# Optimization experiments

Hardware: AMD Instinct MI355X
Metric: run time of the kernel (lower is better)

Reference implementation:

```python
import jax, jax.numpy as jnp
import numpy as np

N_NODES = 50000
N_EDGES = 800000
NUM_GRAPHS = 1024
IN_DIM = 25
DIM = 64
STEPS = 3


def setup_inputs() -> dict:
    key = jax.random.key(0)
    ks = jax.random.split(key, 16)
    s = 0.1
    return {
        "x": jax.random.normal(ks[0], (N_NODES, IN_DIM), dtype=jnp.float32),
        "edge_index": jax.random.randint(ks[1], (2, N_EDGES), 0, N_NODES),
        "batch": jnp.sort(jax.random.randint(ks[2], (N_NODES,), 0, NUM_GRAPHS)),
        "W0": jax.random.normal(ks[3], (IN_DIM, DIM), dtype=jnp.float32) * s,
        "b0": jnp.zeros((DIM,), jnp.float32),
        "Wc": jax.random.normal(ks[4], (DIM, DIM), dtype=jnp.float32) * s,
        "bc": jnp.zeros((DIM,), jnp.float32),
        "Wih": jax.random.normal(ks[5], (4 * DIM, 2 * DIM), dtype=jnp.float32) * s,
        "Whh": jax.random.normal(ks[6], (4 * DIM, DIM), dtype=jnp.float32) * s,
        "bih": jnp.zeros((4 * DIM,), jnp.float32),
        "bhh": jnp.zeros((4 * DIM,), jnp.float32),
        "W1": jax.random.normal(ks[7], (2 * DIM, DIM), dtype=jnp.float32) * s,
        "b1": jnp.zeros((DIM,), jnp.float32),
        "W2": jax.random.normal(ks[8], (DIM, 1), dtype=jnp.float32) * s,
        "b2": jnp.zeros((1,), jnp.float32),
    }


def _lstm_cell(xin, h, c, Wih, Whh, bih, bhh):
    gates = xin @ Wih.T + h @ Whh.T + bih + bhh  # [B, 4*DIM]
    i, f, g, o = jnp.split(gates, 4, axis=-1)
    i, f, o = jax.nn.sigmoid(i), jax.nn.sigmoid(f), jax.nn.sigmoid(o)
    g = jnp.tanh(g)
    c = f * c + i * g
    h = o * jnp.tanh(c)
    return h, c


def reference(x, edge_index, batch, W0, b0, Wc, bc, Wih, Whh, bih, bhh, W1, b1, W2, b2):
    n = x.shape[0]
    # lin0 + relu
    h = jax.nn.relu(x @ W0 + b0)
    # GCNConv: x @ W, add self loops, symmetric normalization, scatter-add
    hw = h @ Wc
    loops = jnp.arange(n, dtype=edge_index.dtype)
    row = jnp.concatenate([edge_index[0], loops])  # sources
    col = jnp.concatenate([edge_index[1], loops])  # targets
    deg = jax.ops.segment_sum(jnp.ones_like(row, dtype=hw.dtype), col, num_segments=n)
    dinv = jnp.where(deg > 0, jax.lax.rsqrt(deg), 0.0)
    norm = dinv[row] * dinv[col]
    msg = hw[row] * norm[:, None]  # [E+N, DIM] gather
    agg = jax.ops.segment_sum(msg, col, num_segments=n) + bc
    h = jax.nn.relu(agg)
    # Set2Set pooling with LSTM, 3 processing steps
    B = NUM_GRAPHS
    q_star = jnp.zeros((B, 2 * DIM), h.dtype)
    hs = jnp.zeros((B, DIM), h.dtype)
    cs = jnp.zeros((B, DIM), h.dtype)
    for _ in range(STEPS):
        hs, cs = _lstm_cell(q_star, hs, cs, Wih, Whh, bih, bhh)
        q = hs  # [B, DIM]
        e = jnp.sum(h * q[batch], axis=-1)  # [N]
        emax = jax.ops.segment_max(e, batch, num_segments=B)
        a = jnp.exp(e - emax[batch])
        asum = jax.ops.segment_sum(a, batch, num_segments=B)
        a = a / asum[batch]
        r = jax.ops.segment_sum(a[:, None] * h, batch, num_segments=B)  # [B, DIM]
        q_star = jnp.concatenate([q, r], axis=-1)
    out = jax.nn.relu(q_star @ W1 + b1)
    out = out @ W2 + b2
    return out.reshape(-1)
```

## Files before the change

### kernel.cpp

```cpp
#include <hip/hip_runtime.h>
#include <hip/hip_fp16.h>
#include <math.h>

#define N_NODES 50000
#define N_EDGES 800000
#define NGRAPH  1024
#define IN_DIM  25
#define DIM     64

#define NBKB 782
#define CAP  1536
#define NBIN 391
#define CROWS 128

__device__ inline float wsum(float v) {
#pragma unroll
  for (int off = 32; off > 0; off >>= 1) v += __shfl_xor(v, off, 64);
  return v;
}
__device__ inline float sigmoidf(float x) { return 1.f / (1.f + expf(-x)); }

__global__ __launch_bounds__(256) void k_bin(const int* __restrict__ ei,
    int* __restrict__ gcur, int* __restrict__ pairs,
    const float* __restrict__ Wih, const float* __restrict__ Whh,
    float* __restrict__ WT) {
  __shared__ int hist[NBKB];
  __shared__ int sbase[NBKB];
  __shared__ int lbase[NBKB];
  __shared__ int sorted[2048];
  int t = threadIdx.x;
  if (blockIdx.x == NBIN) {
    for (int i = t; i < 3 * DIM * 4 * DIM; i += 256) {
      int k = i >> 8, tt = i & 255;
      WT[i] = (k < 2 * DIM) ? Wih[tt * 2 * DIM + k] : Whh[tt * DIM + (k - 2 * DIM)];
    }
    return;
  }
  int base = blockIdx.x * 2048;
  for (int i = t; i < NBKB; i += 256) hist[i] = 0;
  __syncthreads();
  int pk[8], bkt[8], rank[8];
#pragma unroll
  for (int k = 0; k < 8; k++) {
    int e = base + k * 256 + t;
    if (e < N_EDGES) {
      int row = ei[e];
      int col = ei[N_EDGES + e];
      int b = col >> 6;
      bkt[k] = b;
      rank[k] = atomicAdd(&hist[b], 1);
      pk[k] = (int)(((unsigned)b << 22) | ((unsigned)(col & 63) << 16) | (unsigned)row);
    } else {
      bkt[k] = -1;
    }
  }
  __syncthreads();
  if (t < 64) {
    int v[13];
    int loc = 0;
#pragma unroll
    for (int i = 0; i < 13; i++) {
      int idx = t * 13 + i;
      v[i] = (idx < NBKB) ? hist[idx] : 0;
      loc += v[i];
    }
    int x = loc;
#pragma unroll
    for (int d = 1; d < 64; d <<= 1) {
      int y = __shfl_up(x, d, 64);
      if (t >= d) x += y;
    }
    int excl = x - loc;
#pragma unroll
    for (int i = 0; i < 13; i++) {
      int idx = t * 13 + i;
      if (idx < NBKB) sbase[idx] = excl;
      excl += v[i];
    }
  }
  __syncthreads();
#pragma unroll
  for (int k = 0; k < 8; k++)
    if (bkt[k] >= 0) sorted[sbase[bkt[k]] + rank[k]] = pk[k];
  for (int i = t; i < NBKB; i += 256)
    lbase[i] = hist[i] ? atomicAdd(&gcur[i], hist[i]) : 0;
  __syncthreads();
  int ntot = min(2048, N_EDGES - base);
  for (int i = t; i < ntot; i += 256) {
    int p = sorted[i];
    int b = ((unsigned)p) >> 22;
    int gpos = lbase[b] + (i - sbase[b]);
    if (gpos < CAP) pairs[(size_t)b * CAP + gpos] = p & 0x3FFFFF;
  }
}

__global__ __launch_bounds__(256) void k_lin0(const float* __restrict__ x,
    const float* __restrict__ W0, const float* __restrict__ b0,
    const float* __restrict__ Wc, const int* __restrict__ pairs,
    const int* __restrict__ gcur, float* __restrict__ dinv,
    __half* __restrict__ hw16) {
  __shared__ float sx[64][IN_DIM + 1];
  __shared__ float sW0[IN_DIM][DIM];
  __shared__ float sh[64][DIM + 4];
  __shared__ float sWc[DIM][DIM];
  __shared__ int histd[64];
  int t = threadIdx.x;
  int row0 = blockIdx.x * 64;
  if (t < 64) histd[t] = 0;
  __syncthreads();
  for (int i = t; i < 64 * IN_DIM; i += 256) {
    int r = i / IN_DIM, k = i - r * IN_DIM;
    int row = row0 + r;
    sx[r][k] = (row < N_NODES) ? x[row * IN_DIM + k] : 0.f;
  }
  for (int i = t; i < IN_DIM * DIM; i += 256) sW0[i >> 6][i & 63] = W0[i];
  for (int i = t; i < DIM * DIM; i += 256) sWc[i >> 6][i & 63] = Wc[i];
  {
    int ne = min(gcur[blockIdx.x], CAP);
    const int* pp = pairs + (size_t)blockIdx.x * CAP;
    const int4* pp4 = (const int4*)pp;
    int ne4 = ne >> 2;
    for (int i = t; i < ne4; i += 256) {
      int4 p4 = pp4[i];
      atomicAdd(&histd[(p4.x >> 16) & 63], 1);
      atomicAdd(&histd[(p4.y >> 16) & 63], 1);
      atomicAdd(&histd[(p4.z >> 16) & 63], 1);
      atomicAdd(&histd[(p4.w >> 16) & 63], 1);
    }
    for (int i = (ne4 << 2) + t; i < ne; i += 256)
      atomicAdd(&histd[(pp[i] >> 16) & 63], 1);
  }
  __syncthreads();
  int tc = (t & 15) * 4;
  int tr = (t >> 4) * 4;
  float acc[4][4];
  {
    float4 bb = *(const float4*)&b0[tc];
#pragma unroll
    for (int i = 0; i < 4; i++) {
      acc[i][0] = bb.x; acc[i][1] = bb.y; acc[i][2] = bb.z; acc[i][3] = bb.w;
    }
  }
#pragma unroll
  for (int k = 0; k < IN_DIM; k++) {
    float4 w = *(const float4*)&sW0[k][tc];
#pragma unroll
    for (int i = 0; i < 4; i++) {
      float a = sx[tr + i][k];
      acc[i][0] += a * w.x; acc[i][1] += a * w.y;
      acc[i][2] += a * w.z; acc[i][3] += a * w.w;
    }
  }
#pragma unroll
  for (int i = 0; i < 4; i++) {
    sh[tr + i][tc + 0] = fmaxf(acc[i][0], 0.f);
    sh[tr + i][tc + 1] = fmaxf(acc[i][1], 0.f);
    sh[tr + i][tc + 2] = fmaxf(acc[i][2], 0.f);
    sh[tr + i][tc + 3] = fmaxf(acc[i][3], 0.f);
  }
  __syncthreads();
#pragma unroll
  for (int i = 0; i < 4; i++) acc[i][0] = acc[i][1] = acc[i][2] = acc[i][3] = 0.f;
#pragma unroll 8
  for (int k = 0; k < DIM; k++) {
    float4 w = *(const float4*)&sWc[k][tc];
#pragma unroll
    for (int i = 0; i < 4; i++) {
      float a = sh[tr + i][k];
      acc[i][0] += a * w.x; acc[i][1] += a * w.y;
      acc[i][2] += a * w.z; acc[i][3] += a * w.w;
    }
  }
  if (t < 64) {
    int node = row0 + t;
    if (node < N_NODES) dinv[node] = rsqrtf((float)(histd[t] + 1));
  }
  float2* hwf2 = (float2*)hw16;
#pragma unroll
  for (int i = 0; i < 4; i++) {
    int row = row0 + tr + i;
    if (row < N_NODES) {
      float dv = rsqrtf((float)(histd[tr + i] + 1));
      float2 st;
      ((__half2*)&st)[0] = __floats2half2_rn(acc[i][0] * dv, acc[i][1] * dv);
      ((__half2*)&st)[1] = __floats2half2_rn(acc[i][2] * dv, acc[i][3] * dv);
      hwf2[(size_t)row * 16 + (t & 15)] = st;
    }
  }
}

__global__ __launch_bounds__(256) void k_agg(const int* __restrict__ pairs,
    const int* __restrict__ gcur, const __half* __restrict__ hw16,
    const float* __restrict__ dinv, const float4* __restrict__ bc4,
    __half* __restrict__ h16) {
  __shared__ unsigned short rows[CAP];
  __shared__ int hist[64];
  __shared__ int off[65];
  __shared__ int cur[64];
  int b = blockIdx.x, t = threadIdx.x;
  int lane = t & 63, wave = t >> 6, q = lane >> 4, ql = lane & 15;
  int qid = (wave << 2) + q;
  if (t < 64) hist[t] = 0;
  __syncthreads();
  int ne = min(gcur[b], CAP);
  const int* pp = pairs + (size_t)b * CAP;
  const int4* pp4 = (const int4*)pp;
  int ne4 = ne >> 2;
  for (int i = t; i < ne4; i += 256) {
    int4 p4 = pp4[i];
    atomicAdd(&hist[(p4.x >> 16) & 63], 1);
    atomicAdd(&hist[(p4.y >> 16) & 63], 1);
    atomicAdd(&hist[(p4.z >> 16) & 63], 1);
    atomicAdd(&hist[(p4.w >> 16) & 63], 1);
  }
  for (int i = (ne4 << 2) + t; i < ne; i += 256)
    atomicAdd(&hist[(pp[i] >> 16) & 63], 1);
  __syncthreads();
  if (t < 64) {
    int v = hist[t];
    int x = v;
#pragma unroll
    for (int d = 1; d < 64; d <<= 1) {
      int y = __shfl_up(x, d, 64);
      if (t >= d) x += y;
    }
    off[t] = x - v;
    cur[t] = x - v;
    if (t == 63) off[64] = x;
  }
  __syncthreads();
  for (int i = t; i < ne4; i += 256) {
    int4 p4 = pp4[i];
#pragma unroll
    for (int u = 0; u < 4; u++) {
      int p = (&p4.x)[u];
      int slot = atomicAdd(&cur[(p >> 16) & 63], 1);
      rows[slot] = (unsigned short)(p & 0xFFFF);
    }
  }
  for (int i = (ne4 << 2) + t; i < ne; i += 256) {
    int p = pp[i];
    int slot = atomicAdd(&cur[(p >> 16) & 63], 1);
    rows[slot] = (unsigned short)(p & 0xFFFF);
  }
  __syncthreads();
  const float2* hwf2 = (const float2*)hw16;
  float4 bb = bc4[ql];
  for (int nl = qid; nl < 64; nl += 16) {
    int node = b * 64 + nl;
    if (node >= N_NODES) continue;
    int s0 = off[nl], e0 = off[nl + 1];
    float4 a0, a1, a2, a3;
    {
      float2 raw = hwf2[(size_t)node * 16 + ql];
      float2 f0 = __half22float2(((const __half2*)&raw)[0]);
      float2 f1 = __half22float2(((const __half2*)&raw)[1]);
      a0 = make_float4(f0.x, f0.y, f1.x, f1.y);
      a1 = make_float4(0.f, 0.f, 0.f, 0.f); a2 = a1; a3 = a1;
    }
    int j = s0;
    for (; j + 4 <= e0; j += 4) {
      int r0 = rows[j], r1 = rows[j + 1], r2 = rows[j + 2], r3 = rows[j + 3];
      float2 w0 = hwf2[(size_t)r0 * 16 + ql];
      float2 w1 = hwf2[(size_t)r1 * 16 + ql];
      float2 w2 = hwf2[(size_t)r2 * 16 + ql];
      float2 w3 = hwf2[(size_t)r3 * 16 + ql];
      float2 f;
      f = __half22float2(((const __half2*)&w0)[0]); a0.x += f.x; a0.y += f.y;
      f = __half22float2(((const __half2*)&w0)[1]); a0.z += f.x; a0.w += f.y;
      f = __half22float2(((const __half2*)&w1)[0]); a1.x += f.x; a1.y += f.y;
      f = __half22float2(((const __half2*)&w1)[1]); a1.z += f.x; a1.w += f.y;
      f = __half22float2(((const __half2*)&w2)[0]); a2.x += f.x; a2.y += f.y;
      f = __half22float2(((const __half2*)&w2)[1]); a2.z += f.x; a2.w += f.y;
      f = __half22float2(((const __half2*)&w3)[0]); a3.x += f.x; a3.y += f.y;
      f = __half22float2(((const __half2*)&w3)[1]); a3.z += f.x; a3.w += f.y;
    }
    for (; j < e0; j++) {
      int r = rows[j];
      float2 w = hwf2[(size_t)r * 16 + ql];
      float2 f;
      f = __half22float2(((const __half2*)&w)[0]); a0.x += f.x; a0.y += f.y;
      f = __half22float2(((const __half2*)&w)[1]); a0.z += f.x; a0.w += f.y;
    }
    float di = dinv[node];
    float ox = fmaxf(((a0.x + a1.x) + (a2.x + a3.x)) * di + bb.x, 0.f);
    float oy = fmaxf(((a0.y + a1.y) + (a2.y + a3.y)) * di + bb.y, 0.f);
    float oz = fmaxf(((a0.z + a1.z) + (a2.z + a3.z)) * di + bb.z, 0.f);
    float ow = fmaxf(((a0.w + a1.w) + (a2.w + a3.w)) * di + bb.w, 0.f);
    float2 st;
    ((__half2*)&st)[0] = __floats2half2_rn(ox, oy);
    ((__half2*)&st)[1] = __floats2half2_rn(oz, ow);
    ((float2*)h16)[(size_t)node * 16 + ql] = st;
  }
}

__global__ __launch_bounds__(256) void k_set2set(
    const __half* __restrict__ h16, const int* __restrict__ batch,
    const float* __restrict__ WT, const float* __restrict__ bih,
    const float* __restrict__ bhh, const float* __restrict__ W1,
    const float* __restrict__ b1, const float* __restrict__ W2,
    const float* __restrict__ b2, float* __restrict__ out) {
  int b = blockIdx.x, t = threadIdx.x;
  int wave = t >> 6, lane = t & 63;
  int q = lane >> 4, ql = lane & 15;
  int qid = (wave << 2) + q;
  __shared__ float2 hcf2[CROWS * 16];
  __shared__ float qs[2 * DIM];
  __shared__ float hsl[DIM], csl[DIM];
  __shared__ float gates[4 * DIM];
  __shared__ float red[16 * DIM];
  __shared__ float lred[16], wmax[16];
  __shared__ int seg[2];
  const float2* h2 = (const float2*)h16;
  if (t < 2) {
    int g = b + t;
    int lo = 0, hi = N_NODES;
    if (g == NGRAPH) lo = N_NODES;
    else while (lo < hi) { int mid = (lo + hi) >> 1; if (batch[mid] < g) lo = mid + 1; else hi = mid; }
    seg[t] = lo;
  }
  if (t < 2 * DIM) qs[t] = 0.f;
  if (t < DIM) { hsl[t] = 0.f; csl[t] = 0.f; }
  __syncthreads();
  int s = seg[0], eend = seg[1];
  int nc = min(eend - s, CROWS);
  for (int i = t; i < nc * 16; i += 256)
    hcf2[i] = h2[(size_t)(s + (i >> 4)) * 16 + (i & 15)];
  __syncthreads();
  float bsum = bih[t] + bhh[t];
  for (int step = 0; step < 3; step++) {
    float g = bsum;
    if (step > 0) {
      const float* wp = WT + t;
      float g1 = 0.f;
#pragma unroll 8
      for (int k = 0; k < 2 * DIM; k += 2) {
        g += qs[k] * wp[k * 4 * DIM];
        g1 += qs[k + 1] * wp[(k + 1) * 4 * DIM];
      }
#pragma unroll 8
      for (int k = 0; k < DIM; k += 2) {
        g += hsl[k] * wp[(2 * DIM + k) * 4 * DIM];
        g1 += hsl[k + 1] * wp[(2 * DIM + k + 1) * 4 * DIM];
      }
      g += g1;
    }
    gates[t] = g;
    __syncthreads();
    if (t < DIM) {
      float ig = sigmoidf(gates[t]);
      float fg = sigmoidf(gates[DIM + t]);
      float gg = tanhf(gates[2 * DIM + t]);
      float og = sigmoidf(gates[3 * DIM + t]);
      float c = fg * csl[t] + ig * gg;
      csl[t] = c;
      float hh = og * tanhf(c);
      hsl[t] = hh;
      qs[t] = hh;
    }
    __syncthreads();
    float4 qf = *(const float4*)&hsl[4 * ql];
    float m_w = -INFINITY, l_w = 0.f;
    float4 racc = make_float4(0.f, 0.f, 0.f, 0.f);
    for (int j = s + qid; j < eend; j += 16) {
      int lj = j - s;
      float2 raw = (lj < CROWS) ? hcf2[lj * 16 + ql]
                                : h2[(size_t)j * 16 + ql];
      float2 f0 = __half22float2(((const __half2*)&raw)[0]);
      float2 f1 = __half22float2(((const __half2*)&raw)[1]);
      float p = f0.x * qf.x + f0.y * qf.y + f1.x * qf.z + f1.y * qf.w;
#pragma unroll
      for (int off = 1; off < 16; off <<= 1) p += __shfl_xor(p, off, 64);
      float m_new = fmaxf(m_w, p);
      float scale = __expf(m_w - m_new);
      float a = __expf(p - m_new);
      racc.x = racc.x * scale + a * f0.x;
      racc.y = racc.y * scale + a * f0.y;
      racc.z = racc.z * scale + a * f1.x;
      racc.w = racc.w * scale + a * f1.y;
      l_w = l_w * scale + a;
      m_w = m_new;
    }
    *(float4*)&red[qid * DIM + 4 * ql] = racc;
    if (ql == 0) { lred[qid] = l_w; wmax[qid] = m_w; }
    __syncthreads();
    if (t < DIM) {
      float m_b = -1e30f;
      for (int i = 0; i < 16; i++) m_b = fmaxf(m_b, wmax[i]);
      float r = 0.f, l = 0.f;
      for (int i = 0; i < 16; i++) {
        float e = __expf(wmax[i] - m_b);
        r += red[i * DIM + t] * e;
        l += lred[i] * e;
      }
      qs[DIM + t] = (l > 0.f) ? r / l : 0.f;
    }
    __syncthreads();
  }
  if (t < DIM) {
    float acc = b1[t];
#pragma unroll
    for (int k = 0; k < 2 * DIM; k++) acc += qs[k] * W1[k * DIM + t];
    acc = fmaxf(acc, 0.f);
    float v = wsum(acc * W2[t]);
    if (t == 0) out[b] = v + b2[0];
  }
}

extern "C" void kernel_launch(void* const* d_in, const int* in_sizes, int n_in,
                              void* d_out, int out_size, void* d_ws, size_t ws_size,
                              hipStream_t stream) {
  const float* x    = (const float*)d_in[0];
  const int*   ei   = (const int*)d_in[1];
  const int*   batch= (const int*)d_in[2];
  const float* W0   = (const float*)d_in[3];
  const float* b0   = (const float*)d_in[4];
  const float* Wc   = (const float*)d_in[5];
  const float* bc   = (const float*)d_in[6];
  const float* Wih  = (const float*)d_in[7];
  const float* Whh  = (const float*)d_in[8];
  const float* bih  = (const float*)d_in[9];
  const float* bhh  = (const float*)d_in[10];
  const float* W1   = (const float*)d_in[11];
  const float* b1   = (const float*)d_in[12];
  const float* W2   = (const float*)d_in[13];
  const float* b2   = (const float*)d_in[14];
  float* out = (float*)d_out;

  __half* hw16 = (__half*)d_ws;
  __half* h16  = hw16 + (size_t)N_NODES * DIM;
  float* dinv  = (float*)(h16 + (size_t)N_NODES * DIM);
  float* WT    = dinv + N_NODES;
  int* gcur    = (int*)(WT + 3 * DIM * 4 * DIM);
  int* pairs   = gcur + NBKB + 2;

  hipMemsetAsync(gcur, 0, NBKB * sizeof(int), stream);
  k_bin<<<NBIN + 1, 256, 0, stream>>>(ei, gcur, pairs, Wih, Whh, WT);
  k_lin0<<<NBKB, 256, 0, stream>>>(x, W0, b0, Wc, pairs, gcur, dinv, hw16);
  k_agg<<<NBKB, 256, 0, stream>>>(pairs, gcur, hw16, dinv, (const float4*)bc, h16);
  k_set2set<<<NGRAPH, 256, 0, stream>>>(h16, batch, WT, bih, bhh, W1, b1, W2, b2, out);
}
```

Measured before the change: 194.0 us.

## Compute per-node degree with global atomics in binning, drop local sort

The binning kernel now loads edges as int4, counts each target node's degree with global atomics into a new deg array, and writes pairs straight to global slots without the shared-memory local sort. The lin0 and aggregation kernels read deg directly instead of rebuilding histograms from the pairs, which removes one pass over pairs in each. The cost is 800k global atomics on deg, scattered uncoalesced pair writes, and a larger memset. A slot<CAP guard is added in aggregation because the deg-based offsets may not match the capped pair count.

```diff
diff --git a/kernel.cpp b/kernel.cpp
--- a/kernel.cpp
+++ b/kernel.cpp
@@ -21,13 +21,11 @@
 __device__ inline float sigmoidf(float x) { return 1.f / (1.f + expf(-x)); }
 
 __global__ __launch_bounds__(256) void k_bin(const int* __restrict__ ei,
-    int* __restrict__ gcur, int* __restrict__ pairs,
+    int* __restrict__ gcur, int* __restrict__ deg, int* __restrict__ pairs,
     const float* __restrict__ Wih, const float* __restrict__ Whh,
     float* __restrict__ WT) {
   __shared__ int hist[NBKB];
-  __shared__ int sbase[NBKB];
   __shared__ int lbase[NBKB];
-  __shared__ int sorted[2048];
   int t = threadIdx.x;
   if (blockIdx.x == NBIN) {
     for (int i = t; i < 3 * DIM * 4 * DIM; i += 256) {
@@ -39,75 +37,56 @@
   int base = blockIdx.x * 2048;
   for (int i = t; i < NBKB; i += 256) hist[i] = 0;
   __syncthreads();
-  int pk[8], bkt[8], rank[8];
-#pragma unroll
-  for (int k = 0; k < 8; k++) {
-    int e = base + k * 256 + t;
-    if (e < N_EDGES) {
-      int row = ei[e];
-      int col = ei[N_EDGES + e];
-      int b = col >> 6;
-      bkt[k] = b;
-      rank[k] = atomicAdd(&hist[b], 1);
-      pk[k] = (int)(((unsigned)b << 22) | ((unsigned)(col & 63) << 16) | (unsigned)row);
-    } else {
-      bkt[k] = -1;
-    }
-  }
-  __syncthreads();
-  if (t < 64) {
-    int v[13];
-    int loc = 0;
-#pragma unroll
-    for (int i = 0; i < 13; i++) {
-      int idx = t * 13 + i;
-      v[i] = (idx < NBKB) ? hist[idx] : 0;
-      loc += v[i];
-    }
-    int x = loc;
-#pragma unroll
-    for (int d = 1; d < 64; d <<= 1) {
-      int y = __shfl_up(x, d, 64);
-      if (t >= d) x += y;
-    }
-    int excl = x - loc;
-#pragma unroll
-    for (int i = 0; i < 13; i++) {
-      int idx = t * 13 + i;
-      if (idx < NBKB) sbase[idx] = excl;
-      excl += v[i];
-    }
-  }
-  __syncthreads();
-#pragma unroll
-  for (int k = 0; k < 8; k++)
-    if (bkt[k] >= 0) sorted[sbase[bkt[k]] + rank[k]] = pk[k];
+  int n = min(2048, N_EDGES - base);
+  const int4* r4 = (const int4*)(ei + base);
+  const int4* c4 = (const int4*)(ei + N_EDGES + base);
+  int pk[8], rank[8];
+#pragma unroll
+  for (int s = 0; s < 2; s++) {
+    int i = s * 256 + t;
+    int e = i * 4;
+    int4 rv, cv;
+    bool ok = e < n;
+    if (ok) { rv = r4[i]; cv = c4[i]; }
+#pragma unroll
+    for (int u = 0; u < 4; u++) {
+      int k = s * 4 + u;
+      if (ok) {
+        int row = (&rv.x)[u], col = (&cv.x)[u];
+        int b = col >> 6;
+        rank[k] = atomicAdd(&hist[b], 1);
+        atomicAdd(&deg[col], 1);
+        pk[k] = (int)(((unsigned)b << 22) | ((unsigned)(col & 63) << 16) | (unsigned)row);
+      } else {
+        rank[k] = -1;
+      }
+    }
+  }
+  __syncthreads();
   for (int i = t; i < NBKB; i += 256)
     lbase[i] = hist[i] ? atomicAdd(&gcur[i], hist[i]) : 0;
   __syncthreads();
-  int ntot = min(2048, N_EDGES - base);
-  for (int i = t; i < ntot; i += 256) {
-    int p = sorted[i];
-    int b = ((unsigned)p) >> 22;
-    int gpos = lbase[b] + (i - sbase[b]);
-    if (gpos < CAP) pairs[(size_t)b * CAP + gpos] = p & 0x3FFFFF;
+#pragma unroll
+  for (int k = 0; k < 8; k++) {
+    if (rank[k] >= 0) {
+      int b = ((unsigned)pk[k]) >> 22;
+      int pos = lbase[b] + rank[k];
+      if (pos < CAP) pairs[(size_t)b * CAP + pos] = pk[k] & 0x3FFFFF;
+    }
   }
 }
 
 __global__ __launch_bounds__(256) void k_lin0(const float* __restrict__ x,
     const float* __restrict__ W0, const float* __restrict__ b0,
-    const float* __restrict__ Wc, const int* __restrict__ pairs,
-    const int* __restrict__ gcur, float* __restrict__ dinv,
-    __half* __restrict__ hw16) {
+    const float* __restrict__ Wc, const int* __restrict__ deg,
+    float* __restrict__ dinv, __half* __restrict__ hw16) {
   __shared__ float sx[64][IN_DIM + 1];
   __shared__ float sW0[IN_DIM][DIM];
   __shared__ float sh[64][DIM + 4];
   __shared__ float sWc[DIM][DIM];
-  __shared__ int histd[64];
+  __shared__ float sdv[64];
   int t = threadIdx.x;
   int row0 = blockIdx.x * 64;
-  if (t < 64) histd[t] = 0;
-  __syncthreads();
   for (int i = t; i < 64 * IN_DIM; i += 256) {
     int r = i / IN_DIM, k = i - r * IN_DIM;
     int row = row0 + r;
@@ -115,20 +94,11 @@
   }
   for (int i = t; i < IN_DIM * DIM; i += 256) sW0[i >> 6][i & 63] = W0[i];
   for (int i = t; i < DIM * DIM; i += 256) sWc[i >> 6][i & 63] = Wc[i];
-  {
-    int ne = min(gcur[blockIdx.x], CAP);
-    const int* pp = pairs + (size_t)blockIdx.x * CAP;
-    const int4* pp4 = (const int4*)pp;
-    int ne4 = ne >> 2;
-    for (int i = t; i < ne4; i += 256) {
-      int4 p4 = pp4[i];
-      atomicAdd(&histd[(p4.x >> 16) & 63], 1);
-      atomicAdd(&histd[(p4.y >> 16) & 63], 1);
-      atomicAdd(&histd[(p4.z >> 16) & 63], 1);
-      atomicAdd(&histd[(p4.w >> 16) & 63], 1);
-    }
-    for (int i = (ne4 << 2) + t; i < ne; i += 256)
-      atomicAdd(&histd[(pp[i] >> 16) & 63], 1);
+  if (t < 64) {
+    int node = row0 + t;
+    float dv = (node < N_NODES) ? rsqrtf((float)(deg[node] + 1)) : 0.f;
+    sdv[t] = dv;
+    if (node < N_NODES) dinv[node] = dv;
   }
   __syncthreads();
   int tc = (t & 15) * 4;
@@ -171,16 +141,12 @@
       acc[i][2] += a * w.z; acc[i][3] += a * w.w;
     }
   }
-  if (t < 64) {
-    int node = row0 + t;
-    if (node < N_NODES) dinv[node] = rsqrtf((float)(histd[t] + 1));
-  }
   float2* hwf2 = (float2*)hw16;
 #pragma unroll
   for (int i = 0; i < 4; i++) {
     int row = row0 + tr + i;
     if (row < N_NODES) {
-      float dv = rsqrtf((float)(histd[tr + i] + 1));
+      float dv = sdv[tr + i];
       float2 st;
       ((__half2*)&st)[0] = __floats2half2_rn(acc[i][0] * dv, acc[i][1] * dv);
       ((__half2*)&st)[1] = __floats2half2_rn(acc[i][2] * dv, acc[i][3] * dv);
@@ -190,17 +156,28 @@
 }
 
 __global__ __launch_bounds__(256) void k_agg(const int* __restrict__ pairs,
-    const int* __restrict__ gcur, const __half* __restrict__ hw16,
-    const float* __restrict__ dinv, const float4* __restrict__ bc4,
-    __half* __restrict__ h16) {
+    const int* __restrict__ gcur, const int* __restrict__ deg,
+    const __half* __restrict__ hw16, const float* __restrict__ dinv,
+    const float4* __restrict__ bc4, __half* __restrict__ h16) {
   __shared__ unsigned short rows[CAP];
-  __shared__ int hist[64];
   __shared__ int off[65];
   __shared__ int cur[64];
   int b = blockIdx.x, t = threadIdx.x;
   int lane = t & 63, wave = t >> 6, q = lane >> 4, ql = lane & 15;
   int qid = (wave << 2) + q;
-  if (t < 64) hist[t] = 0;
+  if (t < 64) {
+    int node = b * 64 + t;
+    int v = (node < N_NODES) ? deg[node] : 0;
+    int x = v;
+#pragma unroll
+    for (int d = 1; d < 64; d <<= 1) {
+      int y = __shfl_up(x, d, 64);
+      if (t >= d) x += y;
+    }
+    off[t] = x - v;
+    cur[t] = x - v;
+    if (t == 63) off[64] = x;
+  }
   __syncthreads();
   int ne = min(gcur[b], CAP);
   const int* pp = pairs + (size_t)b * CAP;
@@ -208,40 +185,17 @@
   int ne4 = ne >> 2;
   for (int i = t; i < ne4; i += 256) {
     int4 p4 = pp4[i];
-    atomicAdd(&hist[(p4.x >> 16) & 63], 1);
-    atomicAdd(&hist[(p4.y >> 16) & 63], 1);
-    atomicAdd(&hist[(p4.z >> 16) & 63], 1);
-    atomicAdd(&hist[(p4.w >> 16) & 63], 1);
-  }
-  for (int i = (ne4 << 2) + t; i < ne; i += 256)
-    atomicAdd(&hist[(pp[i] >> 16) & 63], 1);
-  __syncthreads();
-  if (t < 64) {
-    int v = hist[t];
-    int x = v;
-#pragma unroll
-    for (int d = 1; d < 64; d <<= 1) {
-      int y = __shfl_up(x, d, 64);
-      if (t >= d) x += y;
-    }
-    off[t] = x - v;
-    cur[t] = x - v;
-    if (t == 63) off[64] = x;
-  }
-  __syncthreads();
-  for (int i = t; i < ne4; i += 256) {
-    int4 p4 = pp4[i];
 #pragma unroll
     for (int u = 0; u < 4; u++) {
       int p = (&p4.x)[u];
       int slot = atomicAdd(&cur[(p >> 16) & 63], 1);
-      rows[slot] = (unsigned short)(p & 0xFFFF);
+      if (slot < CAP) rows[slot] = (unsigned short)(p & 0xFFFF);
     }
   }
   for (int i = (ne4 << 2) + t; i < ne; i += 256) {
     int p = pp[i];
     int slot = atomicAdd(&cur[(p >> 16) & 63], 1);
-    rows[slot] = (unsigned short)(p & 0xFFFF);
+    if (slot < CAP) rows[slot] = (unsigned short)(p & 0xFFFF);
   }
   __syncthreads();
   const float2* hwf2 = (const float2*)hw16;
@@ -432,11 +386,12 @@
   float* dinv  = (float*)(h16 + (size_t)N_NODES * DIM);
   float* WT    = dinv + N_NODES;
   int* gcur    = (int*)(WT + 3 * DIM * 4 * DIM);
-  int* pairs   = gcur + NBKB + 2;
-
-  hipMemsetAsync(gcur, 0, NBKB * sizeof(int), stream);
-  k_bin<<<NBIN + 1, 256, 0, stream>>>(ei, gcur, pairs, Wih, Whh, WT);
-  k_lin0<<<NBKB, 256, 0, stream>>>(x, W0, b0, Wc, pairs, gcur, dinv, hw16);
-  k_agg<<<NBKB, 256, 0, stream>>>(pairs, gcur, hw16, dinv, (const float4*)bc, h16);
+  int* deg     = gcur + NBKB;
+  int* pairs   = deg + N_NODES + 2;
+
+  hipMemsetAsync(gcur, 0, (NBKB + N_NODES) * sizeof(int), stream);
+  k_bin<<<NBIN + 1, 256, 0, stream>>>(ei, gcur, deg, pairs, Wih, Whh, WT);
+  k_lin0<<<NBKB, 256, 0, stream>>>(x, W0, b0, Wc, deg, dinv, hw16);
+  k_agg<<<NBKB, 256, 0, stream>>>(pairs, gcur, deg, hw16, dinv, (const float4*)bc, h16);
   k_set2set<<<NGRAPH, 256, 0, stream>>>(h16, batch, WT, bih, bhh, W1, b1, W2, b2, out);
 }
```

After: 230.5 us. +18.8%, slower.
